# Kernel tuning notes

Measured on AMD Instinct MI355X. Metric: run time of the kernel, lower is better.

Reference implementation:

```python
import jax, jax.numpy as jnp
import numpy as np

C_A = 768; C_S = 384; C_Z = 128; H = 16; D = C_A // H
B = 1; N = 4096; NQ = 32; NK = 128; NB = N // NQ
EPS = 1e-5


def _ln(x):
    # layernorm without learned affine (affine applied by caller where present)
    m = jnp.mean(x, axis=-1, keepdims=True)
    v = jnp.mean((x - m) ** 2, axis=-1, keepdims=True)
    return (x - m) * jax.lax.rsqrt(v + EPS)


def setup_inputs() -> dict:
    key = jax.random.key(0)
    ks = jax.random.split(key, 16)
    w = lambda k, shp: jax.random.normal(k, shp, dtype=jnp.float32) * 0.02
    return dict(
        a=jax.random.normal(ks[0], (B, N, C_A), jnp.float32),
        s=jax.random.normal(ks[1], (B, N, C_S), jnp.float32),
        z=jax.random.normal(ks[2], (B, NB, NQ, NK, C_Z), jnp.float32),
        adaln_gamma_s=jnp.ones((C_S,), jnp.float32),
        adaln_ws=w(ks[3], (C_S, C_A)),
        adaln_bs=jnp.zeros((C_A,), jnp.float32),
        adaln_wskip=w(ks[4], (C_S, C_A)),
        lnz_gamma=jnp.ones((C_Z,), jnp.float32),
        wz=w(ks[5], (C_Z, H)),
        wq=w(ks[6], (C_A, C_A)), bq=jnp.zeros((C_A,), jnp.float32),
        wk=w(ks[7], (C_A, C_A)),
        wv=w(ks[8], (C_A, C_A)),
        wg=w(ks[9], (C_A, C_A)), bg=jnp.ones((C_A,), jnp.float32),
        wo=w(ks[10], (C_A, C_A)), bo=jnp.zeros((C_A,), jnp.float32),
        w_last=w(ks[11], (C_S, C_A)),
        b_last=jnp.full((C_A,), -2.0, jnp.float32),  # biasinit = -2.0
        n_queries=NQ, n_keys=NK,
    )


def _forward(a, s, z, adaln_gamma_s, adaln_ws, adaln_bs, adaln_wskip,
             lnz_gamma, wz, wq, bq, wk, wv, wg, bg, wo, bo,
             w_last, b_last, n_queries, n_keys):
    Bq, Nq, _ = a.shape
    nb = Nq // n_queries
    # AdaptiveLayerNorm (AF3 Alg 26): a <- sigmoid(Lin(s_ln)) * LN(a) + LinNoBias(s_ln)
    s_ln = _ln(s) * adaln_gamma_s
    a_ln = jax.nn.sigmoid(s_ln @ adaln_ws + adaln_bs) * _ln(a) + s_ln @ adaln_wskip
    # pair bias: LN(z) (no offset) -> per-head bias, permuted to [B,H,nb,nq,nk]
    bias = (_ln(z) * lnz_gamma) @ wz                    # [B, nb, nq, nk, H]
    bias = jnp.transpose(bias, (0, 4, 1, 2, 3))          # [B, H, nb, nq, nk]
    # projections (q has bias; k/v no bias)
    q = (a_ln @ wq + bq).reshape(Bq, nb, n_queries, H, D)
    k = (a_ln @ wk).reshape(Bq, Nq, H, D)
    v = (a_ln @ wv).reshape(Bq, Nq, H, D)
    # local window: query block w covers [w*nq, (w+1)*nq); keys are nk centered on it
    start = jnp.arange(nb) * n_queries + n_queries // 2 - n_keys // 2
    kidx = start[:, None] + jnp.arange(n_keys)[None, :]  # [nb, nk]
    valid = (kidx >= 0) & (kidx < Nq)
    kidx = jnp.clip(kidx, 0, Nq - 1)
    k_loc = k[:, kidx]                                    # [B, nb, nk, H, D]
    v_loc = v[:, kidx]
    scale = 1.0 / float(np.sqrt(D))
    scores = jnp.einsum('bwqhd,bwkhd->bhwqk', q, k_loc) * scale + bias
    scores = jnp.where(valid[None, None, :, None, :], scores, -1e9)
    p = jax.nn.softmax(scores, axis=-1)
    o = jnp.einsum('bhwqk,bwkhd->bwqhd', p, v_loc).reshape(Bq, Nq, C_A)
    # gating, output projection, final sigmoid gate from raw s
    o = (jax.nn.sigmoid(a_ln @ wg + bg) * o) @ wo + bo
    return jax.nn.sigmoid(s @ w_last + b_last) * o


def reference(a, s, z, adaln_gamma_s, adaln_ws, adaln_bs, adaln_wskip,
              lnz_gamma, wz, wq, bq, wk, wv, wg, bg, wo, bo,
              w_last, b_last, n_queries, n_keys):
    return _forward(a, s, z, adaln_gamma_s, adaln_ws, adaln_bs, adaln_wskip,
                    lnz_gamma, wz, wq, bq, wk, wv, wg, bg, wo, bo,
                    w_last, b_last, n_queries, n_keys)
```

## Files before the change

kernel.cpp:

```cpp
#include <hip/hip_runtime.h>
#include <hip/hip_bf16.h>
#include <math.h>

#define N_TOK 4096
#define CA 768
#define CS 384
#define CZ 128
#define NHEAD 16
#define DH 48
#define NQW 32
#define NKW 128
#define NBLK 128
#define VT_W 4224

typedef __attribute__((ext_vector_type(8))) short short8;
typedef __attribute__((ext_vector_type(4))) float float4v;
typedef __attribute__((ext_vector_type(4))) unsigned short ushort4v;

__device__ __forceinline__ float sigmoidf_(float x){ return 1.0f/(1.0f+__expf(-x)); }

__device__ __forceinline__ unsigned short f2bf(float x){
  unsigned u = __float_as_uint(x);
  unsigned r = (u + 0x7FFFu + ((u>>16)&1u)) >> 16;
  return (unsigned short)r;
}
__device__ __forceinline__ float bf2f(unsigned short b){
  return __uint_as_float(((unsigned)b)<<16);
}
__device__ __forceinline__ short8 cvt8(const float* xv){
  union { short8 v; unsigned short u[8]; } H;
  #pragma unroll
  for (int j=0;j<8;j++) H.u[j] = f2bf(xv[j]);
  return H.v;
}

__device__ __forceinline__ void gload_lds16(const void* gsrc, void* ldst){
  __builtin_amdgcn_global_load_lds(
    (const __attribute__((address_space(1))) void*)gsrc,
    (__attribute__((address_space(3))) void*)ldst, 16, 0, 0);
}

__global__ __launch_bounds__(256) void prep_kernel(
  const float* __restrict__ s, const float* __restrict__ adaln_gamma,
  unsigned short* __restrict__ s_ln_h, unsigned short* __restrict__ s_h,
  const float* __restrict__ a, float* __restrict__ a_n,
  const float* __restrict__ ws, const float* __restrict__ wskip,
  const float* __restrict__ wq, const float* __restrict__ wk,
  const float* __restrict__ wv, const float* __restrict__ wg,
  const float* __restrict__ wo, const float* __restrict__ wlast,
  unsigned short* __restrict__ Wt1, unsigned short* __restrict__ Wt2,
  unsigned short* __restrict__ Wt3, unsigned short* __restrict__ Wt4,
  const float* __restrict__ bq, const float* __restrict__ bg,
  float* __restrict__ biasq)
{
  __shared__ float tile[64][65];
  int bid = blockIdx.x;
  int tid = threadIdx.x;

  if (bid < 1024){
    int wave = tid>>6, lane = tid&63;
    int row = bid*4 + wave;
    const float* x = s + (size_t)row*CS;
    float v[6]; float sum=0.f, sq=0.f;
    #pragma unroll
    for (int i=0;i<6;i++){ v[i]=x[lane+64*i]; sum+=v[i]; sq+=v[i]*v[i]; }
    #pragma unroll
    for (int off=32; off; off>>=1){ sum+=__shfl_xor(sum,off); sq+=__shfl_xor(sq,off); }
    float m = sum*(1.f/CS);
    float var = sq*(1.f/CS)-m*m;
    float rs = rsqrtf(var+1e-5f);
    #pragma unroll
    for (int i=0;i<6;i++){
      int c = lane+64*i;
      s_ln_h[(size_t)row*CS+c] = f2bf((v[i]-m)*rs*adaln_gamma[c]);
      s_h[(size_t)row*CS+c]    = f2bf(v[i]);
    }
    return;
  }
  bid -= 1024;

  if (bid < 1024){
    int wave = tid>>6, lane = tid&63;
    int row = bid*4 + wave;
    const float* x = a + (size_t)row*CA;
    float v[12]; float sum=0.f, sq=0.f;
    #pragma unroll
    for (int i=0;i<12;i++){ v[i]=x[lane+64*i]; sum+=v[i]; sq+=v[i]*v[i]; }
    #pragma unroll
    for (int off=32; off; off>>=1){ sum+=__shfl_xor(sum,off); sq+=__shfl_xor(sq,off); }
    float m = sum*(1.f/CA);
    float var = sq*(1.f/CA)-m*m;
    float rs = rsqrtf(var+1e-5f);
    float* o = a_n + (size_t)row*CA;
    #pragma unroll
    for (int i=0;i<12;i++) o[lane+64*i] = (v[i]-m)*rs;
    return;
  }
  bid -= 1024;

  if (bid < 936){
    const float* src; unsigned short* dst; int K; int local;
    if      (bid < 72)  { src=ws;    dst=Wt1;                   K=CS; local=bid; }
    else if (bid < 144) { src=wskip; dst=Wt1 + (size_t)768*CS;  K=CS; local=bid-72; }
    else if (bid < 288) { src=wq;    dst=Wt2;                   K=CA; local=bid-144; }
    else if (bid < 432) { src=wk;    dst=Wt2 + (size_t)768*CA;  K=CA; local=bid-288; }
    else if (bid < 576) { src=wv;    dst=Wt2 + (size_t)1536*CA; K=CA; local=bid-432; }
    else if (bid < 720) { src=wg;    dst=Wt2 + (size_t)2304*CA; K=CA; local=bid-576; }
    else if (bid < 864) { src=wo;    dst=Wt3;                   K=CA; local=bid-720; }
    else                { src=wlast; dst=Wt4;                   K=CS; local=bid-864; }
    int ktiles = K/64;
    int kb = (local % ktiles)*64, nb = (local / ktiles)*64;
    int c = tid & 63, r0 = tid >> 6;
    #pragma unroll
    for (int i=0;i<16;i++){
      int r = r0 + 4*i;
      tile[r][c] = src[(size_t)(kb+r)*CA + nb + c];
    }
    __syncthreads();
    #pragma unroll
    for (int i=0;i<16;i++){
      int r = r0 + 4*i;
      dst[(size_t)(nb+r)*K + kb + c] = f2bf(tile[c][r]);
    }
    return;
  }
  bid -= 936;

  int i = bid*256 + tid;
  float v = 0.f;
  if (i < 768) v = bq[i];
  else if (i >= 2304) v = bg[i-2304];
  biasq[i] = v;
}

__global__ __launch_bounds__(256) void zbias_kernel(const float* __restrict__ z,
                                                    const float* __restrict__ gamma,
                                                    const float* __restrict__ wz,
                                                    unsigned short* __restrict__ bias3){
  __shared__ float tbuf[4][16*132];
  int tid = threadIdx.x, wave = tid>>6, lane = tid&63;
  int lr = lane&15, quad = lane>>4;

  short8 bwh[4];
  float w1 = 0.f;
  #pragma unroll
  for (int ks=0;ks<4;ks++){
    float wv[8];
    #pragma unroll
    for (int j=0;j<8;j++){
      int k = ks*32 + quad*8 + j;
      wv[j] = wz[k*NHEAD + lr]*gamma[k];
      w1 += wv[j];
    }
    bwh[ks] = cvt8(wv);
  }
  w1 += __shfl_xor(w1, 16);
  w1 += __shfl_xor(w1, 32);

  size_t group = (size_t)blockIdx.x*4 + wave;
  const float* zg = z + group*(size_t)(NKW*CZ);

  float4 bufA[8], bufB[8];
  auto loadrow = [&](int b, float4* dst){
    const float* zr = zg + (size_t)(b*16 + lr)*CZ + quad*8;
    #pragma unroll
    for (int ks=0;ks<4;ks++){
      dst[ks*2]   = *(const float4*)(zr + ks*32);
      dst[ks*2+1] = *(const float4*)(zr + ks*32 + 4);
    }
  };
  auto process = [&](int b, const float4* d){
    float sum=0.f, sq=0.f;
    #pragma unroll
    for (int p=0;p<8;p++){
      sum += d[p].x + d[p].y + d[p].z + d[p].w;
      sq  += d[p].x*d[p].x + d[p].y*d[p].y + d[p].z*d[p].z + d[p].w*d[p].w;
    }
    sum += __shfl_xor(sum,16); sum += __shfl_xor(sum,32);
    sq  += __shfl_xor(sq,16);  sq  += __shfl_xor(sq,32);
    float mean = sum*(1.f/CZ);
    float var = sq*(1.f/CZ) - mean*mean;
    float rs = rsqrtf(var + 1e-5f);

    float4v c = (float4v){0.f,0.f,0.f,0.f};
    #pragma unroll
    for (int ks=0;ks<4;ks++){
      float xv[8];
      xv[0]=d[ks*2].x;   xv[1]=d[ks*2].y;   xv[2]=d[ks*2].z;   xv[3]=d[ks*2].w;
      xv[4]=d[ks*2+1].x; xv[5]=d[ks*2+1].y; xv[6]=d[ks*2+1].z; xv[7]=d[ks*2+1].w;
      c = __builtin_amdgcn_mfma_f32_16x16x32_bf16(cvt8(xv), bwh[ks], c, 0,0,0);
    }
    #pragma unroll
    for (int r=0;r<4;r++){
      int rrow = quad*4 + r;
      float m_r  = __shfl(mean, rrow);
      float rs_r = __shfl(rs, rrow);
      tbuf[wave][lr*132 + b*16 + rrow] = rs_r*(c[r] - m_r*w1);
    }
  };

  loadrow(0, bufA);
  #pragma unroll 1
  for (int bb=0;bb<4;bb++){
    loadrow(bb*2+1, bufB);
    process(bb*2, bufA);
    if (bb<3) loadrow(bb*2+2, bufA);
    process(bb*2+1, bufB);
  }

  #pragma unroll
  for (int i=0;i<8;i++){
    int h = i*2 + (lane>>5);
    int koff = (lane&31)*4;
    float4 vv = *(const float4*)&tbuf[wave][h*132 + koff];
    ushort4v o4 = { f2bf(vv.x), f2bf(vv.y), f2bf(vv.z), f2bf(vv.w) };
    *(ushort4v*)(bias3 + group*2048 + h*128 + koff) = o4;
  }
}

__global__ __launch_bounds__(256) void adaln_gemm(
  const unsigned short* __restrict__ A, const unsigned short* __restrict__ Bt,
  const float* __restrict__ bs, const float* __restrict__ a_n,
  unsigned short* __restrict__ outh)
{
  __shared__ unsigned short Ash[128*32];
  __shared__ unsigned short B1sh[128*32];
  __shared__ unsigned short B2sh[128*32];

  int tid = threadIdx.x;
  int w = tid >> 6, lane = tid & 63;
  int lr = lane & 15, quad = lane >> 4;
  int m0 = blockIdx.y*128, n0 = blockIdx.x*128;
  int mbase = (w&1)*64, nbase = (w>>1)*64;

  float4v acc1[4][4], acc2[4][4];
  #pragma unroll
  for (int i=0;i<4;i++)
    #pragma unroll
    for (int j=0;j<4;j++){
      acc1[i][j] = (float4v){0.f,0.f,0.f,0.f};
      acc2[i][j] = (float4v){0.f,0.f,0.f,0.f};
    }

  int grow = w*32 + (lane>>2);
  int gcol8 = (lane&3)*8;

  for (int k0=0; k0<CS; k0+=32){
    __syncthreads();
    #pragma unroll
    for (int i=0;i<2;i++){
      int rA = grow + i*16;
      gload_lds16(A  + (size_t)(m0 + rA)*CS + k0 + gcol8, &Ash[(w*32 + i*16)*32]);
      gload_lds16(Bt + (size_t)(n0 + rA)*CS + k0 + gcol8, &B1sh[(w*32 + i*16)*32]);
      gload_lds16(Bt + (size_t)(768 + n0 + rA)*CS + k0 + gcol8, &B2sh[(w*32 + i*16)*32]);
    }
    __syncthreads();

    short8 af[4], b1f[4], b2f[4];
    #pragma unroll
    for (int mi=0;mi<4;mi++)
      af[mi] = *(const short8*)&Ash[(mbase + mi*16 + lr)*32 + quad*8];
    #pragma unroll
    for (int ni=0;ni<4;ni++){
      b1f[ni] = *(const short8*)&B1sh[(nbase + ni*16 + lr)*32 + quad*8];
      b2f[ni] = *(const short8*)&B2sh[(nbase + ni*16 + lr)*32 + quad*8];
    }
    #pragma unroll
    for (int mi=0;mi<4;mi++)
      #pragma unroll
      for (int ni=0;ni<4;ni++){
        acc1[mi][ni] = __builtin_amdgcn_mfma_f32_16x16x32_bf16(af[mi], b1f[ni], acc1[mi][ni], 0,0,0);
        acc2[mi][ni] = __builtin_amdgcn_mfma_f32_16x16x32_bf16(af[mi], b2f[ni], acc2[mi][ni], 0,0,0);
      }
  }

  #pragma unroll
  for (int ni=0;ni<4;ni++){
    int col = n0 + nbase + ni*16 + lr;
    float bsv = bs[col];
    #pragma unroll
    for (int mi=0;mi<4;mi++){
      #pragma unroll
      for (int reg=0;reg<4;reg++){
        int row = m0 + mbase + mi*16 + quad*4 + reg;
        float v = sigmoidf_(acc1[mi][ni][reg] + bsv)*a_n[(size_t)row*CA + col] + acc2[mi][ni][reg];
        outh[(size_t)row*CA + col] = f2bf(v);
      }
    }
  }
}

template<int MODE>
__global__ __launch_bounds__(256) void gemm_bf16(
  const unsigned short* __restrict__ A1, const unsigned short* __restrict__ B1,
  const float* __restrict__ bias1, int K1,
  const unsigned short* __restrict__ A2, const unsigned short* __restrict__ B2,
  const float* __restrict__ bias2, int K2,
  void* __restrict__ outp, int M, int N)
{
  __shared__ unsigned short Ash[128*32];
  __shared__ unsigned short Bsh[128*32];

  int tid = threadIdx.x;
  int w = tid >> 6, lane = tid & 63;
  int lr = lane & 15, quad = lane >> 4;
  int m0 = blockIdx.y*128, n0 = blockIdx.x*128;
  int mbase = (w&1)*64, nbase = (w>>1)*64;

  float4v acc1[4][4];
  float4v acc2[4][4];
  #pragma unroll
  for (int i=0;i<4;i++)
    #pragma unroll
    for (int j=0;j<4;j++){
      acc1[i][j] = (float4v){0.f,0.f,0.f,0.f};
      if constexpr (MODE == 3) acc2[i][j] = (float4v){0.f,0.f,0.f,0.f};
    }

  int grow = w*32 + (lane>>2);
  int gcol8 = (lane&3)*8;

  for (int k0=0; k0<K1; k0+=32){
    __syncthreads();
    #pragma unroll
    for (int i=0;i<2;i++){
      int rA = grow + i*16;
      gload_lds16(A1 + (size_t)(m0 + rA)*K1 + k0 + gcol8, &Ash[(w*32 + i*16)*32]);
      gload_lds16(B1 + (size_t)(n0 + rA)*K1 + k0 + gcol8, &Bsh[(w*32 + i*16)*32]);
    }
    __syncthreads();

    short8 af[4], bf[4];
    #pragma unroll
    for (int mi=0;mi<4;mi++)
      af[mi] = *(const short8*)&Ash[(mbase + mi*16 + lr)*32 + quad*8];
    #pragma unroll
    for (int ni=0;ni<4;ni++)
      bf[ni] = *(const short8*)&Bsh[(nbase + ni*16 + lr)*32 + quad*8];
    #pragma unroll
    for (int mi=0;mi<4;mi++)
      #pragma unroll
      for (int ni=0;ni<4;ni++)
        acc1[mi][ni] = __builtin_amdgcn_mfma_f32_16x16x32_bf16(af[mi], bf[ni], acc1[mi][ni], 0,0,0);
  }

  if constexpr (MODE == 3){
    for (int k0=0; k0<K2; k0+=32){
      __syncthreads();
      #pragma unroll
      for (int i=0;i<2;i++){
        int rA = grow + i*16;
        gload_lds16(A2 + (size_t)(m0 + rA)*K2 + k0 + gcol8, &Ash[(w*32 + i*16)*32]);
        gload_lds16(B2 + (size_t)(n0 + rA)*K2 + k0 + gcol8, &Bsh[(w*32 + i*16)*32]);
      }
      __syncthreads();

      short8 af[4], bf[4];
      #pragma unroll
      for (int mi=0;mi<4;mi++)
        af[mi] = *(const short8*)&Ash[(mbase + mi*16 + lr)*32 + quad*8];
      #pragma unroll
      for (int ni=0;ni<4;ni++)
        bf[ni] = *(const short8*)&Bsh[(nbase + ni*16 + lr)*32 + quad*8];
      #pragma unroll
      for (int mi=0;mi<4;mi++)
        #pragma unroll
        for (int ni=0;ni<4;ni++)
          acc2[mi][ni] = __builtin_amdgcn_mfma_f32_16x16x32_bf16(af[mi], bf[ni], acc2[mi][ni], 0,0,0);
    }
  }

  #pragma unroll
  for (int ni=0;ni<4;ni++){
    int col = n0 + nbase + ni*16 + lr;
    float bv1 = bias1 ? bias1[col] : 0.f;
    float bv2 = (MODE==3 && bias2) ? bias2[col] : 0.f;
    #pragma unroll
    for (int mi=0;mi<4;mi++){
      #pragma unroll
      for (int reg=0;reg<4;reg++){
        int row = m0 + mbase + mi*16 + quad*4 + reg;
        float x1 = acc1[mi][ni][reg] + bv1;
        if constexpr (MODE == 1)
          ((unsigned short*)outp)[(size_t)row*N + col] = f2bf(x1);
        else
          ((float*)outp)[(size_t)row*N + col] = sigmoidf_(acc2[mi][ni][reg] + bv2)*x1;
      }
    }
  }
}

__global__ __launch_bounds__(256) void vtrans_kernel(const unsigned short* __restrict__ qh,
                                                     unsigned short* __restrict__ Vt){
  __shared__ unsigned short tile[64][66];
  int t0 = blockIdx.x*64, c0 = blockIdx.y*64;
  int tid = threadIdx.x;
  int c = tid & 63, r0 = tid >> 6;
  #pragma unroll
  for (int i=0;i<16;i++){
    int r = r0 + 4*i;
    tile[r][c] = qh[(size_t)(t0+r)*3072 + 1536 + c0 + c];
  }
  if (t0 == 0){
    #pragma unroll
    for (int i=0;i<16;i++){
      int r = r0 + 4*i;
      Vt[(size_t)(c0+r)*VT_W + c] = 0;
    }
  } else if (t0 == N_TOK-64){
    #pragma unroll
    for (int i=0;i<16;i++){
      int r = r0 + 4*i;
      Vt[(size_t)(c0+r)*VT_W + 64 + N_TOK + c] = 0;
    }
  }
  __syncthreads();
  #pragma unroll
  for (int i=0;i<16;i++){
    int r = r0 + 4*i;
    Vt[(size_t)(c0+r)*VT_W + 64 + t0 + c] = tile[c][r];
  }
}

__global__ __launch_bounds__(256) void attn_kernel(
  const unsigned short* __restrict__ qh,
  const unsigned short* __restrict__ Vt,
  const unsigned short* __restrict__ bias3h,
  unsigned short* __restrict__ og)
{
  __shared__ unsigned short Pb[4][32*40];
  int tid = threadIdx.x, wave = tid>>6, lane = tid&63;
  int lr = lane&15, quad = lane>>4;
  int w = blockIdx.x, h = blockIdx.y*4 + wave;
  int start = w*NQW - 48;
  const float scale = 0.14433756729740643f;

  short8 zero8 = {0,0,0,0,0,0,0,0};

  short8 aq[2][2];
  #pragma unroll
  for (int mt=0;mt<2;mt++){
    int row = w*NQW + mt*16 + lr;
    const unsigned short* qp = qh + (size_t)row*3072 + h*DH;
    aq[mt][0] = *(const short8*)(qp + quad*8);
    aq[mt][1] = (quad<2) ? *(const short8*)(qp + 32 + quad*8) : zero8;
  }

  float4v c[2][8];
  #pragma unroll
  for (int mt=0;mt<2;mt++)
    #pragma unroll
    for (int nt=0;nt<8;nt++) c[mt][nt] = (float4v){0.f,0.f,0.f,0.f};

  #pragma unroll 1
  for (int nt=0;nt<8;nt++){
    int krc = min(max(start + nt*16 + lr,0),N_TOK-1);
    const unsigned short* kp = qh + (size_t)krc*3072 + 768 + h*DH;
    short8 bk0 = *(const short8*)(kp + quad*8);
    short8 bk1 = (quad<2) ? *(const short8*)(kp + 32 + quad*8) : zero8;
    #pragma unroll
    for (int mt=0;mt<2;mt++){
      c[mt][nt] = __builtin_amdgcn_mfma_f32_16x16x32_bf16(aq[mt][0], bk0, c[mt][nt], 0,0,0);
      c[mt][nt] = __builtin_amdgcn_mfma_f32_16x16x32_bf16(aq[mt][1], bk1, c[mt][nt], 0,0,0);
    }
  }

  float rmax[2][4], rsum[2][4];
  #pragma unroll
  for (int mt=0;mt<2;mt++)
    #pragma unroll
    for (int r=0;r<4;r++){ rmax[mt][r] = -3.0e38f; rsum[mt][r] = 0.f; }

  #pragma unroll
  for (int nt=0;nt<8;nt++){
    int key = start + nt*16 + lr;
    bool valid = (key>=0) && (key<N_TOK);
    #pragma unroll
    for (int mt=0;mt<2;mt++){
      #pragma unroll
      for (int r=0;r<4;r++){
        int q = mt*16 + quad*4 + r;
        float bv = bf2f(bias3h[(((size_t)(w*NQW+q))*NHEAD + h)*128 + nt*16 + lr]);
        float v = valid ? (c[mt][nt][r]*scale + bv) : -1e9f;
        c[mt][nt][r] = v;
        rmax[mt][r] = fmaxf(rmax[mt][r], v);
      }
    }
  }
  #pragma unroll
  for (int mt=0;mt<2;mt++)
    #pragma unroll
    for (int r=0;r<4;r++){
      float m = rmax[mt][r];
      m = fmaxf(m, __shfl_xor(m,1)); m = fmaxf(m, __shfl_xor(m,2));
      m = fmaxf(m, __shfl_xor(m,4)); m = fmaxf(m, __shfl_xor(m,8));
      rmax[mt][r] = m;
    }
  #pragma unroll
  for (int nt=0;nt<8;nt++)
    #pragma unroll
    for (int mt=0;mt<2;mt++)
      #pragma unroll
      for (int r=0;r<4;r++){
        float e = __expf(c[mt][nt][r] - rmax[mt][r]);
        c[mt][nt][r] = e;
        rsum[mt][r] += e;
      }
  #pragma unroll
  for (int mt=0;mt<2;mt++)
    #pragma unroll
    for (int r=0;r<4;r++){
      float sv = rsum[mt][r];
      sv += __shfl_xor(sv,1); sv += __shfl_xor(sv,2);
      sv += __shfl_xor(sv,4); sv += __shfl_xor(sv,8);
      rsum[mt][r] = 1.f/sv;
    }

  unsigned short* ph = &Pb[wave][0];
  float4v o[2][3];
  #pragma unroll
  for (int mt=0;mt<2;mt++)
    #pragma unroll
    for (int no=0;no<3;no++) o[mt][no] = (float4v){0.f,0.f,0.f,0.f};

  #pragma unroll 1
  for (int c2=0;c2<2;c2++){
    #pragma unroll 1
    for (int ks=0;ks<2;ks++){
      int ntb = c2*4 + ks*2;
      #pragma unroll
      for (int t=0;t<2;t++){
        int nt = ntb + t;
        #pragma unroll
        for (int mt=0;mt<2;mt++){
          #pragma unroll
          for (int r=0;r<4;r++){
            int q = mt*16 + quad*4 + r;
            ph[q*40 + t*16 + lr] = f2bf(c[mt][nt][r]*rsum[mt][r]);
          }
        }
      }
      short8 pa[2];
      #pragma unroll
      for (int mt=0;mt<2;mt++)
        pa[mt] = *(const short8*)&ph[(mt*16+lr)*40 + quad*8];
      #pragma unroll
      for (int no=0;no<3;no++){
        int col = h*DH + no*16 + lr;
        const unsigned short* vp = Vt + (size_t)col*VT_W + 64 + start + c2*64 + ks*32 + quad*8;
        short8 bv = *(const short8*)vp;
        #pragma unroll
        for (int mt=0;mt<2;mt++)
          o[mt][no] = __builtin_amdgcn_mfma_f32_16x16x32_bf16(pa[mt], bv, o[mt][no], 0,0,0);
      }
    }
  }

  #pragma unroll
  for (int mt=0;mt<2;mt++){
    #pragma unroll
    for (int no=0;no<3;no++){
      int d = no*16 + lr;
      #pragma unroll
      for (int r=0;r<4;r++){
        int q = mt*16 + quad*4 + r;
        size_t grow = (size_t)(w*NQW + q);
        float g = bf2f(qh[grow*3072 + 2304 + h*DH + d]);
        og[grow*CA + h*DH + d] = f2bf(o[mt][no][r] * sigmoidf_(g));
      }
    }
  }
}

extern "C" void kernel_launch(void* const* d_in, const int* in_sizes, int n_in,
                              void* d_out, int out_size, void* d_ws, size_t ws_size,
                              hipStream_t stream)
{
  const float* a            = (const float*)d_in[0];
  const float* s            = (const float*)d_in[1];
  const float* z            = (const float*)d_in[2];
  const float* adaln_gamma  = (const float*)d_in[3];
  const float* adaln_ws     = (const float*)d_in[4];
  const float* adaln_bs     = (const float*)d_in[5];
  const float* adaln_wskip  = (const float*)d_in[6];
  const float* lnz_gamma    = (const float*)d_in[7];
  const float* wz           = (const float*)d_in[8];
  const float* wq           = (const float*)d_in[9];
  const float* bq           = (const float*)d_in[10];
  const float* wk           = (const float*)d_in[11];
  const float* wv           = (const float*)d_in[12];
  const float* wg           = (const float*)d_in[13];
  const float* bg           = (const float*)d_in[14];
  const float* wo           = (const float*)d_in[15];
  const float* bo           = (const float*)d_in[16];
  const float* w_last       = (const float*)d_in[17];
  const float* b_last       = (const float*)d_in[18];
  float* out = (float*)d_out;

  char* base = (char*)d_ws;
  size_t off = 0;
  auto alloc = [&](size_t bytes)->char*{ char* p = base + off; off += (bytes + 255) & ~(size_t)255; return p; };

  unsigned short* s_ln_h = (unsigned short*)alloc((size_t)N_TOK*CS*2);
  unsigned short* s_h    = (unsigned short*)alloc((size_t)N_TOK*CS*2);
  float*          a_n    = (float*)alloc((size_t)N_TOK*CA*4);
  unsigned short* a_ln_h = (unsigned short*)alloc((size_t)N_TOK*CA*2);
  unsigned short* og_h   = (unsigned short*)alloc((size_t)N_TOK*CA*2);
  unsigned short* Wt1    = (unsigned short*)alloc((size_t)1536*CS*2);
  unsigned short* Wt2    = (unsigned short*)alloc((size_t)3072*CA*2);
  unsigned short* Wt3    = (unsigned short*)alloc((size_t)CA*CA*2);
  unsigned short* Wt4    = (unsigned short*)alloc((size_t)CA*CS*2);
  unsigned short* bias3h = (unsigned short*)alloc((size_t)N_TOK*NHEAD*NKW*2);
  unsigned short* qkvg_h = (unsigned short*)alloc((size_t)N_TOK*3072*2);
  unsigned short* Vt     = (unsigned short*)alloc((size_t)CA*VT_W*2);
  float*          biasq  = (float*)alloc((size_t)3072*4);

  prep_kernel<<<dim3(1024+1024+936+12), 256, 0, stream>>>(
      s, adaln_gamma, s_ln_h, s_h, a, a_n,
      adaln_ws, adaln_wskip, wq, wk, wv, wg, wo, w_last,
      Wt1, Wt2, Wt3, Wt4, bq, bg, biasq);

  zbias_kernel<<<dim3(N_TOK/4), 256, 0, stream>>>(z, lnz_gamma, wz, bias3h);

  adaln_gemm<<<dim3(CA/128, N_TOK/128), 256, 0, stream>>>(s_ln_h, Wt1, adaln_bs, a_n, a_ln_h);

  gemm_bf16<1><<<dim3(3072/128, N_TOK/128), 256, 0, stream>>>(
      a_ln_h, Wt2, biasq, CA, nullptr, nullptr, nullptr, 0, qkvg_h, N_TOK, 3072);

  vtrans_kernel<<<dim3(N_TOK/64, CA/64), 256, 0, stream>>>(qkvg_h, Vt);

  attn_kernel<<<dim3(NBLK, 4), 256, 0, stream>>>(qkvg_h, Vt, bias3h, og_h);

  gemm_bf16<3><<<dim3(CA/128, N_TOK/128), 256, 0, stream>>>(
      og_h, Wt3, bo, CA, s_h, Wt4, b_last, CS, out, N_TOK, CA);
}
```

Before: 234.8 us.

## Stage z via async LDS loads in zbias and prefetch V in attention

```diff
diff --git a/kernel.cpp b/kernel.cpp
--- a/kernel.cpp
+++ b/kernel.cpp
@@ -137,7 +137,7 @@
                                                     const float* __restrict__ gamma,
                                                     const float* __restrict__ wz,
                                                     unsigned short* __restrict__ bias3){
-  __shared__ float tbuf[4][16*132];
+  __shared__ float zbuf[4][2][2048];
   int tid = threadIdx.x, wave = tid>>6, lane = tid&63;
   int lr = lane&15, quad = lane>>4;
 
@@ -159,62 +159,71 @@
 
   size_t group = (size_t)blockIdx.x*4 + wave;
   const float* zg = z + group*(size_t)(NKW*CZ);
-
-  float4 bufA[8], bufB[8];
-  auto loadrow = [&](int b, float4* dst){
-    const float* zr = zg + (size_t)(b*16 + lr)*CZ + quad*8;
+  unsigned short* outg = bias3 + group*2048;
+
+  int rsub = lane>>5;
+  int csw  = lane&31;
+  auto stage = [&](int buf, int b){
+    #pragma unroll
+    for (int i=0;i<8;i++){
+      int r  = 2*i + rsub;
+      int gc = csw ^ (r & 7);
+      gload_lds16(zg + (size_t)(b*16 + r)*CZ + gc*4, &zbuf[wave][buf][i*256]);
+    }
+  };
+
+  stage(0, 0);
+  int buf = 0;
+  #pragma unroll 1
+  for (int b=0; b<8; ++b){
+    if (b < 7){
+      stage(buf^1, b+1);
+      asm volatile("s_waitcnt vmcnt(8)" ::: "memory");
+    } else {
+      asm volatile("s_waitcnt vmcnt(0)" ::: "memory");
+    }
+    __builtin_amdgcn_sched_barrier(0);
+
+    const float* rowp = &zbuf[wave][buf][lr*128];
+    int s = lr & 7;
+    float4 p[8];
     #pragma unroll
     for (int ks=0;ks<4;ks++){
-      dst[ks*2]   = *(const float4*)(zr + ks*32);
-      dst[ks*2+1] = *(const float4*)(zr + ks*32 + 4);
-    }
-  };
-  auto process = [&](int b, const float4* d){
+      int c0 = ks*8 + quad*2;
+      p[ks*2]   = *(const float4*)(rowp + (size_t)((c0  )^s)*4);
+      p[ks*2+1] = *(const float4*)(rowp + (size_t)((c0+1)^s)*4);
+    }
     float sum=0.f, sq=0.f;
     #pragma unroll
-    for (int p=0;p<8;p++){
-      sum += d[p].x + d[p].y + d[p].z + d[p].w;
-      sq  += d[p].x*d[p].x + d[p].y*d[p].y + d[p].z*d[p].z + d[p].w*d[p].w;
+    for (int t=0;t<8;t++){
+      sum += p[t].x + p[t].y + p[t].z + p[t].w;
+      sq  += p[t].x*p[t].x + p[t].y*p[t].y + p[t].z*p[t].z + p[t].w*p[t].w;
     }
     sum += __shfl_xor(sum,16); sum += __shfl_xor(sum,32);
     sq  += __shfl_xor(sq,16);  sq  += __shfl_xor(sq,32);
     float mean = sum*(1.f/CZ);
-    float var = sq*(1.f/CZ) - mean*mean;
+    float var  = sq*(1.f/CZ) - mean*mean;
     float rs = rsqrtf(var + 1e-5f);
 
     float4v c = (float4v){0.f,0.f,0.f,0.f};
     #pragma unroll
     for (int ks=0;ks<4;ks++){
       float xv[8];
-      xv[0]=d[ks*2].x;   xv[1]=d[ks*2].y;   xv[2]=d[ks*2].z;   xv[3]=d[ks*2].w;
-      xv[4]=d[ks*2+1].x; xv[5]=d[ks*2+1].y; xv[6]=d[ks*2+1].z; xv[7]=d[ks*2+1].w;
+      xv[0]=p[ks*2].x;   xv[1]=p[ks*2].y;   xv[2]=p[ks*2].z;   xv[3]=p[ks*2].w;
+      xv[4]=p[ks*2+1].x; xv[5]=p[ks*2+1].y; xv[6]=p[ks*2+1].z; xv[7]=p[ks*2+1].w;
       c = __builtin_amdgcn_mfma_f32_16x16x32_bf16(cvt8(xv), bwh[ks], c, 0,0,0);
     }
+
+    ushort4v o4;
     #pragma unroll
     for (int r=0;r<4;r++){
       int rrow = quad*4 + r;
       float m_r  = __shfl(mean, rrow);
       float rs_r = __shfl(rs, rrow);
-      tbuf[wave][lr*132 + b*16 + rrow] = rs_r*(c[r] - m_r*w1);
-    }
-  };
-
-  loadrow(0, bufA);
-  #pragma unroll 1
-  for (int bb=0;bb<4;bb++){
-    loadrow(bb*2+1, bufB);
-    process(bb*2, bufA);
-    if (bb<3) loadrow(bb*2+2, bufA);
-    process(bb*2+1, bufB);
-  }
-
-  #pragma unroll
-  for (int i=0;i<8;i++){
-    int h = i*2 + (lane>>5);
-    int koff = (lane&31)*4;
-    float4 vv = *(const float4*)&tbuf[wave][h*132 + koff];
-    ushort4v o4 = { f2bf(vv.x), f2bf(vv.y), f2bf(vv.z), f2bf(vv.w) };
-    *(ushort4v*)(bias3 + group*2048 + h*128 + koff) = o4;
+      o4[r] = f2bf(rs_r*(c[r] - m_r*w1));
+    }
+    *(ushort4v*)(outg + lr*128 + b*16 + quad*4) = o4;
+    buf ^= 1;
   }
 }
 
@@ -422,7 +431,7 @@
   }
 }
 
-__global__ __launch_bounds__(256) void attn_kernel(
+__global__ __launch_bounds__(256,2) void attn_kernel(
   const unsigned short* __restrict__ qh,
   const unsigned short* __restrict__ Vt,
   const unsigned short* __restrict__ bias3h,
@@ -452,7 +461,7 @@
     #pragma unroll
     for (int nt=0;nt<8;nt++) c[mt][nt] = (float4v){0.f,0.f,0.f,0.f};
 
-  #pragma unroll 1
+  #pragma unroll 2
   for (int nt=0;nt<8;nt++){
     int krc = min(max(start + nt*16 + lr,0),N_TOK-1);
     const unsigned short* kp = qh + (size_t)krc*3072 + 768 + h*DH;
@@ -464,6 +473,17 @@
       c[mt][nt] = __builtin_amdgcn_mfma_f32_16x16x32_bf16(aq[mt][1], bk1, c[mt][nt], 0,0,0);
     }
   }
+
+  short8 vb[2][2][3];
+  #pragma unroll
+  for (int c2=0;c2<2;c2++)
+    #pragma unroll
+    for (int ks=0;ks<2;ks++)
+      #pragma unroll
+      for (int no=0;no<3;no++){
+        int col = h*DH + no*16 + lr;
+        vb[c2][ks][no] = *(const short8*)(Vt + (size_t)col*VT_W + 64 + start + c2*64 + ks*32 + quad*8);
+      }
 
   float rmax[2][4], rsum[2][4];
   #pragma unroll
@@ -523,9 +543,9 @@
     #pragma unroll
     for (int no=0;no<3;no++) o[mt][no] = (float4v){0.f,0.f,0.f,0.f};
 
-  #pragma unroll 1
+  #pragma unroll
   for (int c2=0;c2<2;c2++){
-    #pragma unroll 1
+    #pragma unroll
     for (int ks=0;ks<2;ks++){
       int ntb = c2*4 + ks*2;
       #pragma unroll
@@ -546,12 +566,9 @@
         pa[mt] = *(const short8*)&ph[(mt*16+lr)*40 + quad*8];
       #pragma unroll
       for (int no=0;no<3;no++){
-        int col = h*DH + no*16 + lr;
-        const unsigned short* vp = Vt + (size_t)col*VT_W + 64 + start + c2*64 + ks*32 + quad*8;
-        short8 bv = *(const short8*)vp;
         #pragma unroll
         for (int mt=0;mt<2;mt++)
-          o[mt][no] = __builtin_amdgcn_mfma_f32_16x16x32_bf16(pa[mt], bv, o[mt][no], 0,0,0);
+          o[mt][no] = __builtin_amdgcn_mfma_f32_16x16x32_bf16(pa[mt], vb[c2][ks][no], o[mt][no], 0,0,0);
       }
     }
   }
```

New measurement: 239.6 us. 2.0% more time.
